# Optimization experiments

Hardware: AMD Instinct MI355X
Metric: run time of the kernel (lower is better)

Reference implementation:

```python
import jax, jax.numpy as jnp
import numpy as np

UNITS = 64

def _tri_indices(u):
    # pairs (a,b) with b>=a in row-major order == tf.boolean_mask(product_mask1)
    pairs = [(a, b) for a in range(u) for b in range(a, u)]
    ia = np.array([p[0] for p in pairs], np.int32)
    ib = np.array([p[1] for p in pairs], np.int32)
    # triples: for product1 index p=(a,b), keep c>=b (derived from mask2 loops)
    ip, ic = [], []
    for p, (a, b) in enumerate(pairs):
        for c in range(b, u):
            ip.append(p)
            ic.append(c)
    return ia, ib, np.array(ip, np.int32), np.array(ic, np.int32)

def setup_inputs() -> dict:
    key = jax.random.key(0)
    k0, k1, k2, k3, k4 = jax.random.split(key, 5)
    B, D, u = 4096, 66, UNITS
    nprod1 = u * (u + 1) // 2            # 2080
    nprod2 = u * (u + 1) * (u + 2) // 6  # 45760
    inputs = jax.random.normal(k0, (B, D), jnp.float32)
    fw1 = jax.random.uniform(k1, (u,), jnp.float32, 0.0, 2.0 * np.pi * 40.0)
    fw2 = jax.random.normal(k2, (u,), jnp.float32) * 0.05
    fb1 = jax.random.normal(k3, (u,), jnp.float32) * 0.05
    wo = jax.random.normal(k4, (u + nprod1 + nprod2, u), jnp.float32) * 0.05
    return {"inputs": inputs, "fw1": fw1, "fw2": fw2, "fb1": fb1, "wo": wo}

def reference(inputs, fw1, fw2, fb1, wo):
    u = fw1.shape[0]
    ia, ib, ip, ic = _tri_indices(u)
    # Fourier features: cos(x * w1 + b1) * w2,  [B, u]
    f = jnp.cos(inputs[:, :u] * fw1 + fb1) * fw2
    # quadratic upper-triangular products, [B, nprod1] (gather instead of dense outer+mask)
    p1 = f[:, ia] * f[:, ib]
    # cubic products c>=b>=a, [B, nprod2]
    p2 = p1[:, ip] * f[:, ic]
    comb = jnp.concatenate([f, p1, p2], axis=1)  # [B, u+nprod1+nprod2]
    pad = jnp.zeros((inputs.shape[0], inputs.shape[1] - u), inputs.dtype)
    return jnp.concatenate([comb @ wo, pad], axis=1) + inputs
```

## Files before the change

### kernel.cpp

```cpp
#include <hip/hip_runtime.h>
#include <hip/hip_bf16.h>

#define NB      4096
#define ND      66
#define NSTEPP  1792
#define KS      64
#define CH      28
#define MB      16
#define FS      72

#define SBLK    NSTEPP
#define FBLK    (NB*FS/256)
#define PBLK    32

typedef __attribute__((ext_vector_type(8))) _Float16 f16x8;
typedef __attribute__((ext_vector_type(4))) _Float16 f16x4;
typedef __attribute__((ext_vector_type(4))) float    f32x4;

__device__ __attribute__((aligned(16))) _Float16 g_f[NB * FS];
__device__ __attribute__((aligned(16))) _Float16 g_woTi[(size_t)(NSTEPP + 1) * 2048];
__device__ __attribute__((aligned(16))) _Float16 g_part[(size_t)KS * MB * 16384];

__constant__ int c_bb[8] = {0, 48, 204, 532, 1096, 1960, 3188, 4844};

__device__ inline unsigned octet_desc(int o) {
    int t = 0;
#pragma unroll
    for (int i = 1; i < 8; ++i) t += (o >= c_bb[i]);
    int li = o - c_bb[t];
    int P = 8 * t + 8, T = P * (P + 1) / 2;
    int s0, s1;
    if (li == 0)       { s0 = 64; s1 = 64; }
    else if (li <= P)  { s0 = li - 1; s1 = 64; }
    else if (li <= P + T) {
        int r = li - P - 1, a = 0;
        while (r >= P - a) { r -= P - a; ++a; }
        s0 = a; s1 = a + r;
    } else             { s0 = 65; s1 = 65; }
    return (unsigned)s0 | ((unsigned)s1 << 8) | ((unsigned)(8 * t) << 16);
}

__global__ void k_prep(const float* __restrict__ inp, const float* __restrict__ fw1,
                       const float* __restrict__ fw2, const float* __restrict__ fb1,
                       const float* __restrict__ wo, float* __restrict__ out) {
    const int bid = blockIdx.x, tid = threadIdx.x;
    if (bid < SBLK) {
        __shared__ unsigned sd[4];
        if (tid < 4) sd[tid] = octet_desc(bid * 4 + tid);
        __syncthreads();
        const int q = tid >> 6, gg = (tid >> 4) & 3, rl = tid & 15;
        const unsigned d = sd[gg];
        const int s0 = d & 255, s1 = (d >> 8) & 255, cb = d >> 16;
        const int n = q * 16 + rl;
        f16x8 v;
        if (s0 == 64) {
#pragma unroll
            for (int j = 0; j < 8; ++j) v[j] = (_Float16)wo[(cb + j) * 64 + n];
        } else if (s0 < 64 && s1 == 64) {
            int base = 64 + s0 * (129 - s0) / 2 + (cb - s0);
#pragma unroll
            for (int j = 0; j < 8; ++j)
                v[j] = (cb + j >= s0) ? (_Float16)wo[(base + j) * 64 + n] : (_Float16)0.f;
        } else if (s0 < 64) {
            int a = s0, b = s1;
            int TP = 45760 - (64 - a) * (65 - a) * (66 - a) / 6;
            int RB = b * (129 - b) / 2 - a * (129 - a) / 2;
            int base = 2144 + TP + RB + (cb - b);
#pragma unroll
            for (int j = 0; j < 8; ++j)
                v[j] = (cb + j >= b) ? (_Float16)wo[(base + j) * 64 + n] : (_Float16)0.f;
        } else {
#pragma unroll
            for (int j = 0; j < 8; ++j) v[j] = (_Float16)0.f;
        }
        *(f16x8*)(g_woTi + (size_t)bid * 2048 + tid * 8) = v;
    } else if (bid < SBLK + FBLK) {
        int i = (bid - SBLK) * 256 + tid;
        int r = i / FS, c = i - r * FS;
        float v;
        if (c < 64)       v = cosf(inp[r * ND + c] * fw1[c] + fb1[c]) * fw2[c];
        else if (c == 64) v = 1.0f;
        else              v = 0.0f;
        g_f[i] = (_Float16)v;
    } else {
        int i = (bid - SBLK - FBLK) * 256 + tid;
        int r = i >> 1, c = 64 + (i & 1);
        out[r * ND + c] = inp[r * ND + c];
    }
}

__global__ __launch_bounds__(128, 2) void k_gemm() {
    __shared__ __attribute__((aligned(16))) _Float16 fl[256 * FS];
    __shared__ __attribute__((aligned(16))) unsigned ldescT[4 * 32];
    const int mb = blockIdx.x, ks = blockIdx.y, tid = threadIdx.x;
    const int s0c = ks * CH;

    {
        const uint4* src = (const uint4*)(g_f + (size_t)mb * 256 * FS);
        uint4* dst = (uint4*)fl;
        for (int e = tid; e < 256 * FS * 2 / 16; e += 128) dst[e] = src[e];
        {
            int gg = tid >> 5, s = tid & 31;
            ldescT[tid] = (s < CH) ? octet_desc((s0c + s) * 4 + gg) : (65u | (65u << 8));
        }
    }
    __syncthreads();

    const int wave = tid >> 6, lane = tid & 63, rl = lane & 15, g = lane >> 4;
    const _Float16* frb = fl + (wave * 128 + rl) * FS;

    f32x4 acc[8][4];
#pragma unroll
    for (int a = 0; a < 8; ++a)
#pragma unroll
        for (int q = 0; q < 4; ++q) acc[a][q] = f32x4{0.f, 0.f, 0.f, 0.f};

    f16x8 cv[8];
    _Float16 fa[8];
#pragma unroll
    for (int a = 0; a < 8; ++a) { cv[a] = f16x8{}; fa[a] = (_Float16)0.f; }
    int cbPrev = -1, siPrev = -1;

    const _Float16* bptr = g_woTi + (size_t)s0c * 2048 + lane * 8;
    f16x8 B0 = *(const f16x8*)(bptr +    0);
    f16x8 B1 = *(const f16x8*)(bptr +  512);
    f16x8 B2 = *(const f16x8*)(bptr + 1024);
    f16x8 B3 = *(const f16x8*)(bptr + 1536);
    bptr += 2048;

#define STEP(dv)                                                               \
    {                                                                          \
        const int si0 = (dv) & 255, si1 = ((dv) >> 8) & 255;                   \
        const int cb = __builtin_amdgcn_readfirstlane((dv) >> 16);             \
        if (__any(si0 != siPrev)) {                                            \
            siPrev = si0;                                                      \
            _Pragma("unroll")                                                  \
            for (int a = 0; a < 8; ++a) fa[a] = frb[a * 16 * FS + si0];        \
        }                                                                      \
        if (cb != cbPrev) {                                                    \
            cbPrev = cb;                                                       \
            _Pragma("unroll")                                                  \
            for (int a = 0; a < 8; ++a)                                        \
                cv[a] = *(const f16x8*)(frb + a * 16 * FS + cb);               \
        }                                                                      \
        f16x8 nB0 = *(const f16x8*)(bptr +    0);                              \
        f16x8 nB1 = *(const f16x8*)(bptr +  512);                              \
        f16x8 nB2 = *(const f16x8*)(bptr + 1024);                              \
        f16x8 nB3 = *(const f16x8*)(bptr + 1536);                              \
        bptr += 2048;                                                          \
        _Pragma("unroll")                                                      \
        for (int a = 0; a < 8; ++a) {                                          \
            const _Float16 p = fa[a] * frb[a * 16 * FS + si1];                 \
            const f16x8 av = cv[a] * p;                                        \
            acc[a][0] = __builtin_amdgcn_mfma_f32_16x16x32_f16(av, B0, acc[a][0], 0, 0, 0); \
            acc[a][1] = __builtin_amdgcn_mfma_f32_16x16x32_f16(av, B1, acc[a][1], 0, 0, 0); \
            acc[a][2] = __builtin_amdgcn_mfma_f32_16x16x32_f16(av, B2, acc[a][2], 0, 0, 0); \
            acc[a][3] = __builtin_amdgcn_mfma_f32_16x16x32_f16(av, B3, acc[a][3], 0, 0, 0); \
        }                                                                      \
        B0 = nB0; B1 = nB1; B2 = nB2; B3 = nB3;                                \
    }

    const unsigned* dT = ldescT + g * 32;
#pragma unroll 1
    for (int s2 = 0; s2 < CH; s2 += 2) {
        uint2 dd = *(const uint2*)(dT + s2);
        STEP(dd.x);
        STEP(dd.y);
    }
#undef STEP

    _Float16* pp = g_part + ((size_t)ks * MB + mb) * 16384 + wave * 8192;
#pragma unroll
    for (int a = 0; a < 8; ++a)
#pragma unroll
        for (int q = 0; q < 4; ++q) {
            f16x4 v;
            v[0] = (_Float16)acc[a][q][0]; v[1] = (_Float16)acc[a][q][1];
            v[2] = (_Float16)acc[a][q][2]; v[3] = (_Float16)acc[a][q][3];
            *(f16x4*)(pp + (a * 4 + q) * 256 + lane * 4) = v;
        }
}

__global__ void k_reduce(const float* __restrict__ inp, float* __restrict__ out) {
    int t = blockIdx.x * 256 + threadIdx.x;
    int c = t & 63, rg = t >> 6;
    int mb = rg >> 6, wave = (rg >> 5) & 1, a = (rg >> 2) & 7, g = rg & 3;
    int q = c >> 4, rl = c & 15, lane = g * 16 + rl;
    int rbase = mb * 256 + wave * 128 + a * 16 + g * 4;
    float acc[4];
#pragma unroll
    for (int i2 = 0; i2 < 4; ++i2) acc[i2] = inp[(rbase + i2) * ND + c];
    const _Float16* pp = g_part + (size_t)mb * 16384 + wave * 8192
                       + (a * 4 + q) * 256 + lane * 4;
#pragma unroll
    for (int ks = 0; ks < KS; ++ks) {
        const f16x4 p = *(const f16x4*)(pp + (size_t)ks * MB * 16384);
#pragma unroll
        for (int i2 = 0; i2 < 4; ++i2) acc[i2] += (float)p[i2];
    }
#pragma unroll
    for (int i2 = 0; i2 < 4; ++i2) out[(rbase + i2) * ND + c] = acc[i2];
}

extern "C" void kernel_launch(void* const* d_in, const int* in_sizes, int n_in,
                              void* d_out, int out_size, void* d_ws, size_t ws_size,
                              hipStream_t stream) {
    const float* inp = (const float*)d_in[0];
    const float* fw1 = (const float*)d_in[1];
    const float* fw2 = (const float*)d_in[2];
    const float* fb1 = (const float*)d_in[3];
    const float* wo  = (const float*)d_in[4];
    float* out = (float*)d_out;

    k_prep<<<SBLK + FBLK + PBLK, 256, 0, stream>>>(inp, fw1, fw2, fb1, wo, out);
    k_gemm<<<dim3(MB, KS), 128, 0, stream>>>();
    k_reduce<<<256, 256, 0, stream>>>(inp, out);
}
```

Measured before the change: 50.16 us.

## Switch GEMM to 32x32x16 MFMA with four waves per block

Replaces the 16x16x32 MFMA tiling with 32x32x16 MFMA instructions. The block grows from two waves of 128 rows each to four waves of 64 rows each, and the packed weight layout, the descriptor table and the reduce-kernel indexing are all re-laid out to match the new fragment shapes. Each step now covers two octets (kstep halves) per MFMA pair and drops the cached first-factor registers, recomputing both factors from LDS per step. The aim is fewer MFMA issues, fewer accumulator registers per wave and more resident waves. The cost is more LDS scalar reads per step and a different occupancy and register balance.

```diff
diff --git a/kernel.cpp b/kernel.cpp
--- a/kernel.cpp
+++ b/kernel.cpp
@@ -13,9 +13,9 @@
 #define FBLK    (NB*FS/256)
 #define PBLK    32
 
-typedef __attribute__((ext_vector_type(8))) _Float16 f16x8;
-typedef __attribute__((ext_vector_type(4))) _Float16 f16x4;
-typedef __attribute__((ext_vector_type(4))) float    f32x4;
+typedef __attribute__((ext_vector_type(8)))  _Float16 f16x8;
+typedef __attribute__((ext_vector_type(4)))  _Float16 f16x4;
+typedef __attribute__((ext_vector_type(16))) float    f32x16;
 
 __device__ __attribute__((aligned(16))) _Float16 g_f[NB * FS];
 __device__ __attribute__((aligned(16))) _Float16 g_woTi[(size_t)(NSTEPP + 1) * 2048];
@@ -48,10 +48,10 @@
         __shared__ unsigned sd[4];
         if (tid < 4) sd[tid] = octet_desc(bid * 4 + tid);
         __syncthreads();
-        const int q = tid >> 6, gg = (tid >> 4) & 3, rl = tid & 15;
-        const unsigned d = sd[gg];
+        const int kstep = tid >> 7, cf = (tid >> 6) & 1, l = tid & 63, h = l >> 5;
+        const unsigned d = sd[kstep * 2 + h];
         const int s0 = d & 255, s1 = (d >> 8) & 255, cb = d >> 16;
-        const int n = q * 16 + rl;
+        const int n = cf * 32 + (l & 31);
         f16x8 v;
         if (s0 == 64) {
 #pragma unroll
@@ -89,109 +89,111 @@
     }
 }
 
-__global__ __launch_bounds__(128, 2) void k_gemm() {
+__global__ __launch_bounds__(256, 4) void k_gemm() {
     __shared__ __attribute__((aligned(16))) _Float16 fl[256 * FS];
-    __shared__ __attribute__((aligned(16))) unsigned ldescT[4 * 32];
+    __shared__ __attribute__((aligned(16))) unsigned ldescT[32 * 4];
     const int mb = blockIdx.x, ks = blockIdx.y, tid = threadIdx.x;
     const int s0c = ks * CH;
 
     {
         const uint4* src = (const uint4*)(g_f + (size_t)mb * 256 * FS);
         uint4* dst = (uint4*)fl;
-        for (int e = tid; e < 256 * FS * 2 / 16; e += 128) dst[e] = src[e];
-        {
-            int gg = tid >> 5, s = tid & 31;
-            ldescT[tid] = (s < CH) ? octet_desc((s0c + s) * 4 + gg) : (65u | (65u << 8));
+        for (int e = tid; e < 256 * FS * 2 / 16; e += 256) dst[e] = src[e];
+        if (tid < 128) {
+            int s = tid >> 2, idx = tid & 3, h = idx >> 1, kst = idx & 1;
+            ldescT[tid] = (s < CH) ? octet_desc((s0c + s) * 4 + kst * 2 + h)
+                                   : (65u | (65u << 8));
         }
     }
     __syncthreads();
 
-    const int wave = tid >> 6, lane = tid & 63, rl = lane & 15, g = lane >> 4;
-    const _Float16* frb = fl + (wave * 128 + rl) * FS;
-
-    f32x4 acc[8][4];
-#pragma unroll
-    for (int a = 0; a < 8; ++a)
-#pragma unroll
-        for (int q = 0; q < 4; ++q) acc[a][q] = f32x4{0.f, 0.f, 0.f, 0.f};
-
-    f16x8 cv[8];
-    _Float16 fa[8];
-#pragma unroll
-    for (int a = 0; a < 8; ++a) { cv[a] = f16x8{}; fa[a] = (_Float16)0.f; }
-    int cbPrev = -1, siPrev = -1;
+    const int wave = tid >> 6, lane = tid & 63, h = lane >> 5, rl = lane & 31;
+    const _Float16* fr0 = fl + (wave * 64 + rl) * FS;
+    const _Float16* fr1 = fr0 + 32 * FS;
+
+    f32x16 acc[2][2];
+#pragma unroll
+    for (int rf = 0; rf < 2; ++rf)
+#pragma unroll
+        for (int cf = 0; cf < 2; ++cf)
+#pragma unroll
+            for (int i = 0; i < 16; ++i) acc[rf][cf][i] = 0.f;
+
+    f16x8 cv0{}, cv1{};
+    int cbPrev = -1;
 
     const _Float16* bptr = g_woTi + (size_t)s0c * 2048 + lane * 8;
-    f16x8 B0 = *(const f16x8*)(bptr +    0);
-    f16x8 B1 = *(const f16x8*)(bptr +  512);
-    f16x8 B2 = *(const f16x8*)(bptr + 1024);
-    f16x8 B3 = *(const f16x8*)(bptr + 1536);
+    f16x8 B00 = *(const f16x8*)(bptr +    0);
+    f16x8 B01 = *(const f16x8*)(bptr +  512);
+    f16x8 B10 = *(const f16x8*)(bptr + 1024);
+    f16x8 B11 = *(const f16x8*)(bptr + 1536);
     bptr += 2048;
 
-#define STEP(dv)                                                               \
-    {                                                                          \
-        const int si0 = (dv) & 255, si1 = ((dv) >> 8) & 255;                   \
-        const int cb = __builtin_amdgcn_readfirstlane((dv) >> 16);             \
-        if (__any(si0 != siPrev)) {                                            \
-            siPrev = si0;                                                      \
-            _Pragma("unroll")                                                  \
-            for (int a = 0; a < 8; ++a) fa[a] = frb[a * 16 * FS + si0];        \
-        }                                                                      \
-        if (cb != cbPrev) {                                                    \
-            cbPrev = cb;                                                       \
-            _Pragma("unroll")                                                  \
-            for (int a = 0; a < 8; ++a)                                        \
-                cv[a] = *(const f16x8*)(frb + a * 16 * FS + cb);               \
-        }                                                                      \
-        f16x8 nB0 = *(const f16x8*)(bptr +    0);                              \
-        f16x8 nB1 = *(const f16x8*)(bptr +  512);                              \
-        f16x8 nB2 = *(const f16x8*)(bptr + 1024);                              \
-        f16x8 nB3 = *(const f16x8*)(bptr + 1536);                              \
-        bptr += 2048;                                                          \
-        _Pragma("unroll")                                                      \
-        for (int a = 0; a < 8; ++a) {                                          \
-            const _Float16 p = fa[a] * frb[a * 16 * FS + si1];                 \
-            const f16x8 av = cv[a] * p;                                        \
-            acc[a][0] = __builtin_amdgcn_mfma_f32_16x16x32_f16(av, B0, acc[a][0], 0, 0, 0); \
-            acc[a][1] = __builtin_amdgcn_mfma_f32_16x16x32_f16(av, B1, acc[a][1], 0, 0, 0); \
-            acc[a][2] = __builtin_amdgcn_mfma_f32_16x16x32_f16(av, B2, acc[a][2], 0, 0, 0); \
-            acc[a][3] = __builtin_amdgcn_mfma_f32_16x16x32_f16(av, B3, acc[a][3], 0, 0, 0); \
-        }                                                                      \
-        B0 = nB0; B1 = nB1; B2 = nB2; B3 = nB3;                                \
-    }
-
-    const unsigned* dT = ldescT + g * 32;
 #pragma unroll 1
-    for (int s2 = 0; s2 < CH; s2 += 2) {
-        uint2 dd = *(const uint2*)(dT + s2);
-        STEP(dd.x);
-        STEP(dd.y);
-    }
-#undef STEP
-
-    _Float16* pp = g_part + ((size_t)ks * MB + mb) * 16384 + wave * 8192;
-#pragma unroll
-    for (int a = 0; a < 8; ++a)
-#pragma unroll
-        for (int q = 0; q < 4; ++q) {
-            f16x4 v;
-            v[0] = (_Float16)acc[a][q][0]; v[1] = (_Float16)acc[a][q][1];
-            v[2] = (_Float16)acc[a][q][2]; v[3] = (_Float16)acc[a][q][3];
-            *(f16x4*)(pp + (a * 4 + q) * 256 + lane * 4) = v;
+    for (int s = 0; s < CH; ++s) {
+        const uint2 dd = *(const uint2*)(&ldescT[s * 4 + h * 2]);
+        const int cb = __builtin_amdgcn_readfirstlane(dd.x >> 16);
+        if (cb != cbPrev) {
+            cbPrev = cb;
+            cv0 = *(const f16x8*)(fr0 + cb);
+            cv1 = *(const f16x8*)(fr1 + cb);
         }
+        f16x8 nB00 = *(const f16x8*)(bptr +    0);
+        f16x8 nB01 = *(const f16x8*)(bptr +  512);
+        f16x8 nB10 = *(const f16x8*)(bptr + 1024);
+        f16x8 nB11 = *(const f16x8*)(bptr + 1536);
+        bptr += 2048;
+
+        const int si00 = dd.x & 255, si01 = (dd.x >> 8) & 255;
+        const int si10 = dd.y & 255, si11 = (dd.y >> 8) & 255;
+        const _Float16 p00 = fr0[si00] * fr0[si01];
+        const _Float16 p10 = fr1[si00] * fr1[si01];
+        const _Float16 p01 = fr0[si10] * fr0[si11];
+        const _Float16 p11 = fr1[si10] * fr1[si11];
+
+        const f16x8 a00 = cv0 * p00, a10 = cv1 * p10;
+        acc[0][0] = __builtin_amdgcn_mfma_f32_32x32x16_f16(a00, B00, acc[0][0], 0, 0, 0);
+        acc[0][1] = __builtin_amdgcn_mfma_f32_32x32x16_f16(a00, B01, acc[0][1], 0, 0, 0);
+        acc[1][0] = __builtin_amdgcn_mfma_f32_32x32x16_f16(a10, B00, acc[1][0], 0, 0, 0);
+        acc[1][1] = __builtin_amdgcn_mfma_f32_32x32x16_f16(a10, B01, acc[1][1], 0, 0, 0);
+
+        const f16x8 a01 = cv0 * p01, a11 = cv1 * p11;
+        acc[0][0] = __builtin_amdgcn_mfma_f32_32x32x16_f16(a01, B10, acc[0][0], 0, 0, 0);
+        acc[0][1] = __builtin_amdgcn_mfma_f32_32x32x16_f16(a01, B11, acc[0][1], 0, 0, 0);
+        acc[1][0] = __builtin_amdgcn_mfma_f32_32x32x16_f16(a11, B10, acc[1][0], 0, 0, 0);
+        acc[1][1] = __builtin_amdgcn_mfma_f32_32x32x16_f16(a11, B11, acc[1][1], 0, 0, 0);
+
+        B00 = nB00; B01 = nB01; B10 = nB10; B11 = nB11;
+    }
+
+    _Float16* pp = g_part + ((size_t)ks * MB + mb) * 16384 + wave * 4096;
+#pragma unroll
+    for (int rf = 0; rf < 2; ++rf)
+#pragma unroll
+        for (int cf = 0; cf < 2; ++cf)
+#pragma unroll
+            for (int rg = 0; rg < 4; ++rg) {
+                f16x4 v;
+                v[0] = (_Float16)acc[rf][cf][rg * 4 + 0];
+                v[1] = (_Float16)acc[rf][cf][rg * 4 + 1];
+                v[2] = (_Float16)acc[rf][cf][rg * 4 + 2];
+                v[3] = (_Float16)acc[rf][cf][rg * 4 + 3];
+                *(f16x4*)(pp + ((cf * 2 + rf) * 4 + rg) * 256 + lane * 4) = v;
+            }
 }
 
 __global__ void k_reduce(const float* __restrict__ inp, float* __restrict__ out) {
     int t = blockIdx.x * 256 + threadIdx.x;
-    int c = t & 63, rg = t >> 6;
-    int mb = rg >> 6, wave = (rg >> 5) & 1, a = (rg >> 2) & 7, g = rg & 3;
-    int q = c >> 4, rl = c & 15, lane = g * 16 + rl;
-    int rbase = mb * 256 + wave * 128 + a * 16 + g * 4;
+    int l = t & 63, grp = t >> 6;
+    int mb = grp >> 6, wave = (grp >> 4) & 3, cf = (grp >> 3) & 1,
+        rf = (grp >> 2) & 1, rg = grp & 3;
+    int rbase = mb * 256 + wave * 64 + rf * 32 + 8 * rg + 4 * (l >> 5);
+    int col = cf * 32 + (l & 31);
     float acc[4];
 #pragma unroll
-    for (int i2 = 0; i2 < 4; ++i2) acc[i2] = inp[(rbase + i2) * ND + c];
-    const _Float16* pp = g_part + (size_t)mb * 16384 + wave * 8192
-                       + (a * 4 + q) * 256 + lane * 4;
+    for (int i2 = 0; i2 < 4; ++i2) acc[i2] = inp[(rbase + i2) * ND + col];
+    const _Float16* pp = g_part + (size_t)mb * 16384 + wave * 4096
+                       + ((cf * 2 + rf) * 4 + rg) * 256 + l * 4;
 #pragma unroll
     for (int ks = 0; ks < KS; ++ks) {
         const f16x4 p = *(const f16x4*)(pp + (size_t)ks * MB * 16384);
@@ -199,7 +201,7 @@
         for (int i2 = 0; i2 < 4; ++i2) acc[i2] += (float)p[i2];
     }
 #pragma unroll
-    for (int i2 = 0; i2 < 4; ++i2) out[(rbase + i2) * ND + c] = acc[i2];
+    for (int i2 = 0; i2 < 4; ++i2) out[(rbase + i2) * ND + col] = acc[i2];
 }
 
 extern "C" void kernel_launch(void* const* d_in, const int* in_sizes, int n_in,
@@ -213,6 +215,6 @@
     float* out = (float*)d_out;
 
     k_prep<<<SBLK + FBLK + PBLK, 256, 0, stream>>>(inp, fw1, fw2, fb1, wo, out);
-    k_gemm<<<dim3(MB, KS), 128, 0, stream>>>();
+    k_gemm<<<dim3(MB, KS), 256, 0, stream>>>();
     k_reduce<<<256, 256, 0, stream>>>(inp, out);
 }
```

New measurement: 53.85 us. 7.3% more time.
